# Performance work log

Measured on AMD Instinct MI355X. Metric: run time of the kernel, lower is better.

The kernel has to match this reference:

```python
import jax, jax.numpy as jnp
import numpy as np


def _build_R(angles, mus):
    """Build n x n orthonormal matrix from n(n-1)/2 Givens angles, then scale rows by mus.
    Rotation order matches SaivDr's OrthonormalMatrixGenerationSystem: iTop outer, iBtm inner.
    """
    n = mus.shape[0]
    top_np, btm_np = np.triu_indices(n, k=1)  # row-major pair order (0,1),(0,2),...,(n-2,n-1)
    top = jnp.asarray(top_np, dtype=jnp.int32)
    btm = jnp.asarray(btm_np, dtype=jnp.int32)
    c = jnp.cos(angles)
    s = jnp.sin(angles)

    def step(R, cstb):
        ci, si, t, b = cstb
        rt = R[t]
        rb = R[b]
        R = R.at[t].set(ci * rt - si * rb)
        R = R.at[b].set(si * rt + ci * rb)
        return R, None

    R0 = jnp.eye(n, dtype=angles.dtype)
    R, _ = jax.lax.scan(step, R0, (c, s, top, btm))
    return mus[:, None] * R


def setup_inputs() -> dict:
    key = jax.random.key(0)
    k1, k2 = jax.random.split(key)
    n, m = 64, 1_000_000
    X = jax.random.normal(k1, (n, m), dtype=jnp.float32)
    angles = jax.random.normal(k2, (n * (n - 1) // 2,), dtype=jnp.float32)
    mus = jnp.ones((n,), dtype=jnp.float32)
    return {"X": X, "angles": angles, "mus": mus}


def reference(X, angles, mus):
    # OrthonormalTransform, mode='Analysis': out = R @ X
    R = _build_R(angles, mus)
    return R @ X
```

## Files before the change

### kernel.cpp

```cpp
#include <hip/hip_runtime.h>
#include <math.h>

#define N 64
#define NPAIRS (N * (N - 1) / 2)

__global__ __launch_bounds__(64) void build_r_kernel(
    const float* __restrict__ angles, const float* __restrict__ mus,
    float* __restrict__ RT) {
  __shared__ float2 cs[NPAIRS];
  const int lane = threadIdx.x;

  for (int k = lane; k < NPAIRS; k += 64) {
    float a = angles[k];
    float s, c;
    sincosf(a, &s, &c);
    cs[k] = make_float2(c, s);
  }
  __syncthreads();

  float col[N];
#pragma unroll
  for (int i = 0; i < N; ++i) col[i] = (i == lane) ? 1.0f : 0.0f;

  int k = 0;
#pragma unroll
  for (int t = 0; t < N - 1; ++t) {
#pragma unroll
    for (int b = t + 1; b < N; ++b) {
      float2 p = cs[k++];
      float rt = col[t];
      float rb = col[b];
      col[t] = fmaf(p.x, rt, -p.y * rb);
      col[b] = fmaf(p.y, rt, p.x * rb);
    }
  }

#pragma unroll
  for (int i = 0; i < N; ++i) {
    RT[lane * N + i] = mus[i] * col[i];
  }
}

__global__ __launch_bounds__(256) void apply_r_kernel(
    const float* __restrict__ X, const float* __restrict__ RT,
    float* __restrict__ out, int m) {
  const int j = blockIdx.x * 256 + threadIdx.x;
  if (j >= m) return;

  float acc[N];
#pragma unroll
  for (int i = 0; i < N; ++i) acc[i] = 0.0f;

  const float* xp = X + j;
#pragma unroll 4
  for (int k = 0; k < N; ++k) {
    const float x = xp[(size_t)k * m];
    const float4* r4 = (const float4*)(RT + k * N);
#pragma unroll
    for (int ii = 0; ii < N / 4; ++ii) {
      float4 r = r4[ii];
      acc[ii * 4 + 0] = fmaf(r.x, x, acc[ii * 4 + 0]);
      acc[ii * 4 + 1] = fmaf(r.y, x, acc[ii * 4 + 1]);
      acc[ii * 4 + 2] = fmaf(r.z, x, acc[ii * 4 + 2]);
      acc[ii * 4 + 3] = fmaf(r.w, x, acc[ii * 4 + 3]);
    }
  }

#pragma unroll
  for (int i = 0; i < N; ++i) {
    out[(size_t)i * m + j] = acc[i];
  }
}

extern "C" void kernel_launch(void* const* d_in, const int* in_sizes, int n_in,
                              void* d_out, int out_size, void* d_ws,
                              size_t ws_size, hipStream_t stream) {
  const float* X = (const float*)d_in[0];
  const float* angles = (const float*)d_in[1];
  const float* mus = (const float*)d_in[2];
  float* out = (float*)d_out;
  float* RT = (float*)d_ws;

  const int m = in_sizes[0] / N;

  build_r_kernel<<<1, 64, 0, stream>>>(angles, mus, RT);

  const int blocks = (m + 255) / 256;
  apply_r_kernel<<<blocks, 256, 0, stream>>>(X, RT, out, m);
}
```

Before: 487.3 us.

## Parallelize Givens build across 8 waves and stage R in shared memory

The R-building kernel now splits the 2016 Givens rotations into 8 segments, one per wavefront. Each segment's partial matrix is then combined by shared-memory matrix products, which shortens the serial single-wave rotation chain. The apply kernel copies R into LDS once per block instead of reading it from global/scalar memory, unrolls the k loop more, and uses nontemporal loads and stores for X and out to avoid cache pollution. In exchange the build kernel adds 7 chained 64x64 matmuls with several barriers, and LDS reads replace what may have been uniform scalar loads.

```diff
diff --git a/kernel.cpp b/kernel.cpp
--- a/kernel.cpp
+++ b/kernel.cpp
@@ -3,17 +3,43 @@
 
 #define N 64
 #define NPAIRS (N * (N - 1) / 2)
+#define NSEG 8
+#define SEGLEN (NPAIRS / NSEG)
+#define STJ 68
 
-__global__ __launch_bounds__(64) void build_r_kernel(
+template <int LO, int HI>
+__device__ __forceinline__ void apply_seg(float col[N], const float2* cs) {
+  int k = 0;
+#pragma unroll
+  for (int t = 0; t < N - 1; ++t) {
+#pragma unroll
+    for (int b = t + 1; b < N; ++b) {
+      if (k >= LO && k < HI) {
+        float2 p = cs[k];
+        float rt = col[t];
+        float rb = col[b];
+        col[t] = fmaf(p.x, rt, -p.y * rb);
+        col[b] = fmaf(p.y, rt, p.x * rb);
+      }
+      ++k;
+    }
+  }
+}
+
+__global__ __launch_bounds__(512) void build_r_kernel(
     const float* __restrict__ angles, const float* __restrict__ mus,
     float* __restrict__ RT) {
   __shared__ float2 cs[NPAIRS];
-  const int lane = threadIdx.x;
+  __shared__ float P[N * N];
+  __shared__ float ST[N * STJ];
 
-  for (int k = lane; k < NPAIRS; k += 64) {
-    float a = angles[k];
+  const int tid = threadIdx.x;
+  const int lane = tid & 63;
+  const int wid = tid >> 6;
+
+  for (int k = tid; k < NPAIRS; k += 512) {
     float s, c;
-    sincosf(a, &s, &c);
+    sincosf(angles[k], &s, &c);
     cs[k] = make_float2(c, s);
   }
   __syncthreads();
@@ -22,29 +48,82 @@
 #pragma unroll
   for (int i = 0; i < N; ++i) col[i] = (i == lane) ? 1.0f : 0.0f;
 
-  int k = 0;
+  switch (wid) {
+    case 0: apply_seg<0 * SEGLEN, 1 * SEGLEN>(col, cs); break;
+    case 1: apply_seg<1 * SEGLEN, 2 * SEGLEN>(col, cs); break;
+    case 2: apply_seg<2 * SEGLEN, 3 * SEGLEN>(col, cs); break;
+    case 3: apply_seg<3 * SEGLEN, 4 * SEGLEN>(col, cs); break;
+    case 4: apply_seg<4 * SEGLEN, 5 * SEGLEN>(col, cs); break;
+    case 5: apply_seg<5 * SEGLEN, 6 * SEGLEN>(col, cs); break;
+    case 6: apply_seg<6 * SEGLEN, 7 * SEGLEN>(col, cs); break;
+    case 7: apply_seg<7 * SEGLEN, 8 * SEGLEN>(col, cs); break;
+  }
+
+  if (wid == 0) {
 #pragma unroll
-  for (int t = 0; t < N - 1; ++t) {
+    for (int i = 0; i < N; ++i) P[i * N + lane] = col[i];
+  }
+  __syncthreads();
+
+  const int i0 = wid * 8;
+  float acc[8];
 #pragma unroll
-    for (int b = t + 1; b < N; ++b) {
-      float2 p = cs[k++];
-      float rt = col[t];
-      float rb = col[b];
-      col[t] = fmaf(p.x, rt, -p.y * rb);
-      col[b] = fmaf(p.y, rt, p.x * rb);
+  for (int u = 0; u < 8; ++u) acc[u] = 0.0f;
+
+  for (int w = 1; w < NSEG; ++w) {
+    if (wid == w) {
+#pragma unroll
+      for (int u = 0; u < N / 4; ++u) {
+        *(float4*)&ST[lane * STJ + u * 4] =
+            make_float4(col[4 * u], col[4 * u + 1], col[4 * u + 2], col[4 * u + 3]);
+      }
     }
+    __syncthreads();
+
+#pragma unroll
+    for (int u = 0; u < 8; ++u) acc[u] = 0.0f;
+#pragma unroll 4
+    for (int k = 0; k < N; ++k) {
+      float bkj = P[k * N + lane];
+      float4 a0 = *(const float4*)&ST[k * STJ + i0];
+      float4 a1 = *(const float4*)&ST[k * STJ + i0 + 4];
+      acc[0] = fmaf(a0.x, bkj, acc[0]);
+      acc[1] = fmaf(a0.y, bkj, acc[1]);
+      acc[2] = fmaf(a0.z, bkj, acc[2]);
+      acc[3] = fmaf(a0.w, bkj, acc[3]);
+      acc[4] = fmaf(a1.x, bkj, acc[4]);
+      acc[5] = fmaf(a1.y, bkj, acc[5]);
+      acc[6] = fmaf(a1.z, bkj, acc[6]);
+      acc[7] = fmaf(a1.w, bkj, acc[7]);
+    }
+    __syncthreads();
+#pragma unroll
+    for (int u = 0; u < 8; ++u) P[(i0 + u) * N + lane] = acc[u];
+    __syncthreads();
   }
 
 #pragma unroll
-  for (int i = 0; i < N; ++i) {
-    RT[lane * N + i] = mus[i] * col[i];
+  for (int u = 0; u < 8; ++u) {
+    const int i = i0 + u;
+    RT[lane * N + i] = mus[i] * acc[u];
   }
 }
 
 __global__ __launch_bounds__(256) void apply_r_kernel(
     const float* __restrict__ X, const float* __restrict__ RT,
     float* __restrict__ out, int m) {
-  const int j = blockIdx.x * 256 + threadIdx.x;
+  __shared__ float Rs[N * N];
+
+  const int tid = threadIdx.x;
+  {
+    const float4* __restrict__ src = (const float4*)RT;
+    float4* dst = (float4*)Rs;
+#pragma unroll
+    for (int u = 0; u < 4; ++u) dst[u * 256 + tid] = src[u * 256 + tid];
+  }
+  __syncthreads();
+
+  const int j = blockIdx.x * 256 + tid;
   if (j >= m) return;
 
   float acc[N];
@@ -52,10 +131,10 @@
   for (int i = 0; i < N; ++i) acc[i] = 0.0f;
 
   const float* xp = X + j;
-#pragma unroll 4
+#pragma unroll 8
   for (int k = 0; k < N; ++k) {
-    const float x = xp[(size_t)k * m];
-    const float4* r4 = (const float4*)(RT + k * N);
+    const float x = __builtin_nontemporal_load(xp + (size_t)k * m);
+    const float4* r4 = (const float4*)(Rs + k * N);
 #pragma unroll
     for (int ii = 0; ii < N / 4; ++ii) {
       float4 r = r4[ii];
@@ -68,7 +147,7 @@
 
 #pragma unroll
   for (int i = 0; i < N; ++i) {
-    out[(size_t)i * m + j] = acc[i];
+    __builtin_nontemporal_store(acc[i], out + (size_t)i * m + j);
   }
 }
 
@@ -83,7 +162,7 @@
 
   const int m = in_sizes[0] / N;
 
-  build_r_kernel<<<1, 64, 0, stream>>>(angles, mus, RT);
+  build_r_kernel<<<1, 512, 0, stream>>>(angles, mus, RT);
 
   const int blocks = (m + 255) / 256;
   apply_r_kernel<<<blocks, 256, 0, stream>>>(X, RT, out, m);
```

New measurement: 659.9 us. 1.35x slower.
